# Kernel optimization log

Hardware: AMD Instinct MI355X
Metric: run time of the kernel (lower is better)

## Reference

```python
import jax, jax.numpy as jnp
import numpy as np

WINDOW = 8
HEADS = 16
HIDDEN = 256
EMBED = HIDDEN * WINDOW          # 2048
HEAD_DIM = EMBED // HEADS        # 128
BATCH = 8
SEQ = 4096                       # multiple of WINDOW
GROUP = SEQ // WINDOW            # 512


def _indices():
    # index_one[i*g + j] = j*w + i  (residue-class grouping permutation)
    i = np.arange(WINDOW)
    j = np.arange(GROUP)
    index_one = (j[None, :] * WINDOW + i[:, None]).reshape(-1)
    # index_two[i*w + k] = k*g + i  (inverse-style interleave permutation)
    index_two = (np.arange(WINDOW)[None, :] * GROUP + np.arange(GROUP)[:, None]).reshape(-1)
    return jnp.asarray(index_one), jnp.asarray(index_two)


def _attention(M, Wq, Wk, Wv, fc_w, fc_b):
    # M: [N, g, E] with E = heads*head_dim
    N, L, E = M.shape
    x = M.reshape(N, L, HEADS, HEAD_DIM)
    q = jnp.einsum('nlhd,ed->nlhe', x, Wq)
    k = jnp.einsum('nlhd,ed->nlhe', x, Wk)
    v = jnp.einsum('nlhd,ed->nlhe', x, Wv)
    energy = jnp.einsum('nqhd,nkhd->nhqk', q, k)
    attn = jax.nn.softmax(energy / jnp.sqrt(jnp.float32(EMBED)), axis=-1)
    out = jnp.einsum('nhqk,nkhd->nqhd', attn, v).reshape(N, L, E)
    return out @ fc_w.T + fc_b


def setup_inputs() -> dict:
    key = jax.random.key(0)
    ks = jax.random.split(key, 6)
    s = 0.02
    return {
        'M': jax.random.normal(ks[0], (BATCH, SEQ, HIDDEN), jnp.float32),
        'Wq': jax.random.normal(ks[1], (HEAD_DIM, HEAD_DIM), jnp.float32) * s,
        'Wk': jax.random.normal(ks[2], (HEAD_DIM, HEAD_DIM), jnp.float32) * s,
        'Wv': jax.random.normal(ks[3], (HEAD_DIM, HEAD_DIM), jnp.float32) * s,
        'fc_w': jax.random.normal(ks[4], (EMBED, EMBED), jnp.float32) * s,
        'fc_b': jax.random.normal(ks[5], (EMBED,), jnp.float32) * s,
        'device': 0,
    }


def reference(M, Wq, Wk, Wv, fc_w, fc_b, device):
    del device  # unused, mirrors torch signature
    index_one, index_two = _indices()
    N, S, H = M.shape
    w, g = WINDOW, GROUP
    for b in range(w):
        idx = (index_one - b) % S
        M = M[:, idx]                                             # gather permute
        # segmentation step 1: [N, w*g, H] -> [N, g, w*H]
        M = M.reshape(N, w, g, H).transpose(0, 2, 1, 3).reshape(N, g, w * H)
        M = _attention(M, Wq, Wk, Wv, fc_w, fc_b)
        # segmentation step 2: [N, g, w*H] -> [N, w*g, H]
        M = M.reshape(N, g, w, H).transpose(0, 2, 1, 3).reshape(N, w * g, H)
        # index_two rotated once per iteration after the first -> roll by -b
        M = M[:, jnp.roll(index_two, -b)]
    return M[:, :S]
```

## Files before the change

### kernel.cpp

```cpp
#include <hip/hip_runtime.h>
#include <stdint.h>

typedef unsigned short u16;
typedef unsigned int u32;
typedef __bf16 bf16x8 __attribute__((ext_vector_type(8)));
typedef float f32x4 __attribute__((ext_vector_type(4)));
typedef float f32x16 __attribute__((ext_vector_type(16)));
typedef u16 u16x4 __attribute__((ext_vector_type(4)));
typedef u16 u16x8 __attribute__((ext_vector_type(8)));

#define MFMA16(a, b, c) __builtin_amdgcn_mfma_f32_16x16x32_bf16(a, b, c, 0, 0, 0)
#define MFMA32(a, b, c) __builtin_amdgcn_mfma_f32_32x32x16_bf16(a, b, c, 0, 0, 0)

__device__ __forceinline__ u16 f2bf(float f) {
  u32 u = __builtin_bit_cast(u32, f);
  u += 0x7FFFu + ((u >> 16) & 1u);
  return (u16)(u >> 16);
}

__device__ __forceinline__ bf16x8 ld16(const u16* p) {
  return __builtin_bit_cast(bf16x8, *(const uint4*)p);
}

__device__ __forceinline__ void gl_lds(const u16* src, u16* lds) {
  __builtin_amdgcn_global_load_lds(
      (const __attribute__((address_space(1))) u32*)src,
      (__attribute__((address_space(3))) u32*)lds, 16, 0, 0);
}

__global__ __launch_bounds__(256) void convert_weights(
    const float* __restrict__ Wq, const float* __restrict__ Wk,
    const float* __restrict__ Wv, const float* __restrict__ fcw,
    u16* __restrict__ wq_b, u16* __restrict__ wk_b, u16* __restrict__ wv_b,
    u16* __restrict__ fcw_b) {
  int bx = blockIdx.x, tid = threadIdx.x;
  if (bx < 4096) {
    int i = (bx * 256 + tid) * 4;
    float4 f = *(const float4*)&fcw[i];
    u16x4 o = {f2bf(f.x), f2bf(f.y), f2bf(f.z), f2bf(f.w)};
    *(u16x4*)&fcw_b[i] = o;
  } else {
    int i = ((bx - 4096) * 256 + tid) * 4;
    const float sc = 0.022097086912079612f;
    float4 q = *(const float4*)&Wq[i];
    u16x4 oq = {f2bf(q.x * sc), f2bf(q.y * sc), f2bf(q.z * sc), f2bf(q.w * sc)};
    *(u16x4*)&wq_b[i] = oq;
    float4 k = *(const float4*)&Wk[i];
    u16x4 ok = {f2bf(k.x), f2bf(k.y), f2bf(k.z), f2bf(k.w)};
    *(u16x4*)&wk_b[i] = ok;
    float4 v = *(const float4*)&Wv[i];
    u16x4 ov = {f2bf(v.x), f2bf(v.y), f2bf(v.z), f2bf(v.w)};
    *(u16x4*)&wv_b[i] = ov;
  }
}

__global__ __launch_bounds__(384) void qkv_kernel(
    const float* __restrict__ src, const u16* __restrict__ wq,
    const u16* __restrict__ wk, const u16* __restrict__ wvw,
    u16* __restrict__ Q, u16* __restrict__ K, u16* __restrict__ Vt, int bsh) {
  __shared__ u16 X[64 * 136];
  int jt = blockIdx.x, h = blockIdx.y, n = blockIdx.z;
  int tid = threadIdx.x;
  int i0 = h >> 1, c0 = (h & 1) * 128;
  for (int it = 0; it < 3; ++it) {
    int c = tid + it * 384;
    if (c < 1024) {
      int row = c >> 4, seg = c & 15;
      int j = jt * 64 + row;
      int pos = (8 * j + i0 - bsh) & 4095;
      const float* g = src + ((size_t)n * 4096 + pos) * 256 + c0 + seg * 8;
      float4 f0 = *(const float4*)g;
      float4 f1 = *(const float4*)(g + 4);
      u16x8 v = {f2bf(f0.x), f2bf(f0.y), f2bf(f0.z), f2bf(f0.w),
                 f2bf(f1.x), f2bf(f1.y), f2bf(f1.z), f2bf(f1.w)};
      *(u16x8*)&X[row * 136 + seg * 8] = v;
    }
  }
  __syncthreads();
  int wv = tid >> 6, ln = tid & 63;
  int mat = wv >> 1;
  int cbase = (wv & 1) * 64;
  const u16* W = (mat == 0) ? wq : (mat == 1) ? wk : wvw;
  int lr = ln & 15, lg = ln >> 4;
  f32x4 acc[4][4] = {};
#pragma unroll
  for (int kt = 0; kt < 4; ++kt) {
    bf16x8 a[4], b[4];
#pragma unroll
    for (int mt = 0; mt < 4; ++mt)
      a[mt] = ld16(&X[(mt * 16 + lr) * 136 + kt * 32 + lg * 8]);
#pragma unroll
    for (int nc = 0; nc < 4; ++nc)
      b[nc] = ld16(&W[(cbase + nc * 16 + lr) * 128 + kt * 32 + lg * 8]);
#pragma unroll
    for (int mt = 0; mt < 4; ++mt)
#pragma unroll
      for (int nc = 0; nc < 4; ++nc)
        acc[mt][nc] = MFMA16(a[mt], b[nc], acc[mt][nc]);
  }
  size_t nh = (size_t)(n * 16 + h);
  if (mat < 2) {
    u16* dst = (mat == 0 ? Q : K) + nh * 512 * 128;
#pragma unroll
    for (int mt = 0; mt < 4; ++mt)
#pragma unroll
      for (int nc = 0; nc < 4; ++nc) {
        int col = cbase + nc * 16 + lr;
        int jb = jt * 64 + mt * 16 + lg * 4;
#pragma unroll
        for (int r = 0; r < 4; ++r)
          dst[(size_t)(jb + r) * 128 + col] = f2bf(acc[mt][nc][r]);
      }
  } else {
    u16* dst = Vt + nh * 128 * 512;
#pragma unroll
    for (int mt = 0; mt < 4; ++mt)
#pragma unroll
      for (int nc = 0; nc < 4; ++nc) {
        int col = cbase + nc * 16 + lr;
        int jb = jt * 64 + mt * 16 + lg * 4;
        u16x4 pk = {f2bf(acc[mt][nc][0]), f2bf(acc[mt][nc][1]),
                    f2bf(acc[mt][nc][2]), f2bf(acc[mt][nc][3])};
        *(u16x4*)&dst[(size_t)col * 512 + jb] = pk;
      }
  }
}

__global__ __launch_bounds__(256, 2) void attn_kernel(
    const u16* __restrict__ Q, const u16* __restrict__ K,
    const u16* __restrict__ Vt, u16* __restrict__ O) {
  __shared__ u16 KL[2][64 * 128];
  __shared__ u16 VL[2][128 * 64];
  int flat = blockIdx.x;
  int xcd = flat & 7, idx = flat >> 3;
  int gl = idx & 15, qt = idx >> 4;
  int g = xcd | (gl << 3);
  int h = g & 15, n = g >> 4;
  int tid = threadIdx.x, wv = tid >> 6, ln = tid & 63;
  int l31 = ln & 31, hh = ln >> 5;
  size_t nh = (size_t)(n * 16 + h);
  int q0 = qt * 128 + wv * 32;
  const u16* Qb = Q + ((size_t)nh * 512 + q0) * 128;
  const u16* Kb = K + (size_t)nh * 512 * 128;
  const u16* Vb = Vt + (size_t)nh * 128 * 512;

  bf16x8 qf[8];
#pragma unroll
  for (int kt = 0; kt < 8; ++kt)
    qf[kt] = ld16(&Qb[l31 * 128 + kt * 16 + hh * 8]);

  int l16 = ln & 15, l8 = ln & 7;
  int rK[4], cK[4], rV[4], cV[4];
#pragma unroll
  for (int i = 0; i < 4; ++i) {
    int s = wv * 4 + i;
    rK[i] = 4 * s + (ln >> 4);
    cK[i] = (l16 ^ (rK[i] & 15)) * 8;
    rV[i] = 8 * s + (ln >> 3);
    cV[i] = (l8 ^ (rV[i] & 7)) * 8;
  }

#pragma unroll
  for (int i = 0; i < 4; ++i) {
    int s = wv * 4 + i;
    gl_lds(&Kb[(size_t)rK[i] * 128 + cK[i]], &KL[0][s * 512]);
    gl_lds(&Vb[(size_t)rV[i] * 512 + 0 * 64 + cV[i]], &VL[0][s * 512]);
  }
  __syncthreads();

  f32x16 o[4] = {};
  float m = -1e30f, l = 0.f;

  for (int kv = 0; kv < 8; ++kv) {
    int cur = kv & 1;
    if (kv < 7) {
      int nxt = cur ^ 1;
      const u16* kp = Kb + (size_t)(kv + 1) * 64 * 128;
#pragma unroll
      for (int i = 0; i < 4; ++i) {
        int s = wv * 4 + i;
        gl_lds(&kp[(size_t)rK[i] * 128 + cK[i]], &KL[nxt][s * 512]);
        gl_lds(&Vb[(size_t)rV[i] * 512 + (kv + 1) * 64 + cV[i]], &VL[nxt][s * 512]);
      }
    }
    f32x16 s[2] = {};
#pragma unroll
    for (int kb = 0; kb < 2; ++kb)
#pragma unroll
      for (int kt = 0; kt < 8; ++kt) {
        int row = kb * 32 + l31;
        int slot = (2 * kt + hh) ^ (row & 15);
        bf16x8 a = ld16(&KL[cur][row * 128 + slot * 8]);
        s[kb] = MFMA32(a, qf[kt], s[kb]);
      }
    float mx[8];
#pragma unroll
    for (int i = 0; i < 8; ++i)
      mx[i] = fmaxf(fmaxf(s[0][2 * i], s[0][2 * i + 1]),
                    fmaxf(s[1][2 * i], s[1][2 * i + 1]));
    float pm = fmaxf(fmaxf(fmaxf(mx[0], mx[1]), fmaxf(mx[2], mx[3])),
                     fmaxf(fmaxf(mx[4], mx[5]), fmaxf(mx[6], mx[7])));
    pm = fmaxf(pm, __shfl_xor(pm, 32));
    if (!__all(pm <= m + 8.f)) {
      float nm = fmaxf(m, pm);
      float al = __expf(m - nm);
      l *= al;
      m = nm;
#pragma unroll
      for (int r = 0; r < 16; ++r) {
        int qr = (r & 3) + 8 * (r >> 2) + 4 * hh;
        float av = __shfl(al, (ln & 32) | qr, 64);
        o[0][r] *= av; o[1][r] *= av; o[2][r] *= av; o[3][r] *= av;
      }
    }
#pragma unroll
    for (int kb = 0; kb < 2; ++kb)
#pragma unroll
      for (int r = 0; r < 16; ++r) s[kb][r] = __expf(s[kb][r] - m);
    float sm[8];
#pragma unroll
    for (int i = 0; i < 8; ++i)
      sm[i] = (s[0][2 * i] + s[0][2 * i + 1]) + (s[1][2 * i] + s[1][2 * i + 1]);
    float rs = ((sm[0] + sm[1]) + (sm[2] + sm[3])) +
               ((sm[4] + sm[5]) + (sm[6] + sm[7]));
    rs += __shfl_xor(rs, 32);
    l += rs;
    bf16x8 pa[4];
#pragma unroll
    for (int ks = 0; ks < 4; ++ks) {
      const int kb = ks >> 1, r0 = 8 * (ks & 1);
      u32 wA, wB, wC, wD;
      asm("v_cvt_pk_bf16_f32 %0, %1, %2" : "=v"(wA) : "v"(s[kb][r0 + 0]), "v"(s[kb][r0 + 1]));
      asm("v_cvt_pk_bf16_f32 %0, %1, %2" : "=v"(wB) : "v"(s[kb][r0 + 2]), "v"(s[kb][r0 + 3]));
      asm("v_cvt_pk_bf16_f32 %0, %1, %2" : "=v"(wC) : "v"(s[kb][r0 + 4]), "v"(s[kb][r0 + 5]));
      asm("v_cvt_pk_bf16_f32 %0, %1, %2" : "=v"(wD) : "v"(s[kb][r0 + 6]), "v"(s[kb][r0 + 7]));
      asm("v_permlane32_swap_b32 %0, %1" : "+v"(wA), "+v"(wC));
      asm("v_permlane32_swap_b32 %0, %1" : "+v"(wB), "+v"(wD));
      uint4 ww = {wA, wB, wC, wD};
      pa[ks] = __builtin_bit_cast(bf16x8, ww);
    }
#pragma unroll
    for (int ks = 0; ks < 4; ++ks)
#pragma unroll
      for (int nb = 0; nb < 4; ++nb) {
        int row = nb * 32 + l31;
        int slot = (2 * ks + hh) ^ (row & 7);
        bf16x8 bv = ld16(&VL[cur][row * 64 + slot * 8]);
        o[nb] = MFMA32(pa[ks], bv, o[nb]);
      }
    if (kv < 7) __syncthreads();
  }
  float inv = 1.f / l;
#pragma unroll
  for (int r = 0; r < 16; ++r) {
    int qr = (r & 3) + 8 * (r >> 2) + 4 * hh;
    float iv = __shfl(inv, (ln & 32) | qr, 64);
    int row = q0 + qr;
    u16* dst = O + ((size_t)n * 512 + row) * 2048 + h * 128;
    dst[0 * 32 + l31] = f2bf(o[0][r] * iv);
    dst[1 * 32 + l31] = f2bf(o[1][r] * iv);
    dst[2 * 32 + l31] = f2bf(o[2][r] * iv);
    dst[3 * 32 + l31] = f2bf(o[3][r] * iv);
  }
}

__global__ __launch_bounds__(256) void fc_kernel(
    const u16* __restrict__ A, const u16* __restrict__ Bw,
    const float* __restrict__ bias, float* __restrict__ dout, int bsh) {
  __shared__ u16 Al[128 * 32];
  __shared__ u16 Bl[128 * 32];
  int bn = blockIdx.x, bm = blockIdx.y;
  int tid = threadIdx.x, wv = tid >> 6, ln = tid & 63;
  int lr = ln & 15, lg = ln >> 4;
  int R0 = bm * 128, C0 = bn * 128;
  int wr = (wv & 1) * 64, wc = (wv >> 1) * 64;
  int lrow = ln >> 2, lseg = ln & 3;
  f32x4 acc[4][4] = {};
  for (int ks = 0; ks < 64; ++ks) {
    int k0 = ks * 32;
#pragma unroll
    for (int ch = wv; ch < 8; ch += 4) {
      const u16* ga = A + (size_t)(R0 + ch * 16 + lrow) * 2048 + k0 + lseg * 8;
      gl_lds(ga, &Al[ch * 512]);
      const u16* gb = Bw + (size_t)(C0 + ch * 16 + lrow) * 2048 + k0 + lseg * 8;
      gl_lds(gb, &Bl[ch * 512]);
    }
    __syncthreads();
    bf16x8 a[4], b[4];
#pragma unroll
    for (int mt = 0; mt < 4; ++mt)
      a[mt] = ld16(&Al[(wr + mt * 16 + lr) * 32 + lg * 8]);
#pragma unroll
    for (int nc = 0; nc < 4; ++nc)
      b[nc] = ld16(&Bl[(wc + nc * 16 + lr) * 32 + lg * 8]);
#pragma unroll
    for (int mt = 0; mt < 4; ++mt)
#pragma unroll
      for (int nc = 0; nc < 4; ++nc)
        acc[mt][nc] = MFMA16(a[mt], b[nc], acc[mt][nc]);
    __syncthreads();
  }
#pragma unroll
  for (int nc = 0; nc < 4; ++nc) {
    int e = C0 + wc + nc * 16 + lr;
    float bv = bias[e];
    int i = e >> 8, cc = e & 255;
#pragma unroll
    for (int mt = 0; mt < 4; ++mt)
#pragma unroll
      for (int r = 0; r < 4; ++r) {
        int row = R0 + wr + mt * 16 + lg * 4 + r;
        int nn = row >> 9, j = row & 511;
        int pos = (8 * j + i - bsh) & 4095;
        dout[((size_t)nn * 4096 + pos) * 256 + cc] = acc[mt][nc][r] + bv;
      }
  }
}

extern "C" void kernel_launch(void* const* d_in, const int* in_sizes, int n_in,
                              void* d_out, int out_size, void* d_ws, size_t ws_size,
                              hipStream_t stream) {
  const float* M = (const float*)d_in[0];
  const float* Wq = (const float*)d_in[1];
  const float* Wk = (const float*)d_in[2];
  const float* Wv = (const float*)d_in[3];
  const float* fcw = (const float*)d_in[4];
  const float* fcb = (const float*)d_in[5];
  float* out = (float*)d_out;
  char* ws = (char*)d_ws;
  u16* wq_b = (u16*)(ws + (0 << 10));
  u16* wk_b = (u16*)(ws + (32 << 10));
  u16* wv_b = (u16*)(ws + (64 << 10));
  u16* fcw_b = (u16*)(ws + (128 << 10));
  u16* Qb = (u16*)(ws + ((size_t)16 << 20));
  u16* Kb = (u16*)(ws + ((size_t)32 << 20));
  u16* Vtb = (u16*)(ws + ((size_t)48 << 20));
  u16* Ab = (u16*)(ws + ((size_t)64 << 20));

  convert_weights<<<4112, 256, 0, stream>>>(Wq, Wk, Wv, fcw, wq_b, wk_b, wv_b, fcw_b);
  for (int b = 0; b < 8; ++b) {
    const float* src = (b == 0) ? M : out;
    qkv_kernel<<<dim3(8, 16, 8), 384, 0, stream>>>(src, wq_b, wk_b, wv_b, Qb, Kb, Vtb, b);
    attn_kernel<<<512, 256, 0, stream>>>(Qb, Kb, Vtb, Ab);
    fc_kernel<<<dim3(16, 32), 256, 0, stream>>>(Ab, fcw_b, fcb, out, b);
  }
}
```

Measured before the change: 810.0 us.

## Double-buffer FC GEMM with larger tiles, merge QKV head pairs, add MFMA priorities

The FC GEMM kernel now uses 512-thread blocks with 128x256 tiles. It double-buffers LDS with swizzled layouts and splits each k-step into two phases with partial vmcnt waits, so global loads overlap MFMA work. The QKV kernel processes both heads of a row residue in one 768-thread block, loading the full 256-wide row once instead of twice. s_setprio hints are also added around MFMA sections in attention and FC. These changes trade more LDS and register pressure, and more complex barrier ordering, for fewer redundant loads and better latency hiding.

```diff
diff --git a/kernel.cpp b/kernel.cpp
--- a/kernel.cpp
+++ b/kernel.cpp
@@ -54,32 +54,29 @@
   }
 }
 
-__global__ __launch_bounds__(384) void qkv_kernel(
+__global__ __launch_bounds__(768) void qkv_kernel(
     const float* __restrict__ src, const u16* __restrict__ wq,
     const u16* __restrict__ wk, const u16* __restrict__ wvw,
     u16* __restrict__ Q, u16* __restrict__ K, u16* __restrict__ Vt, int bsh) {
-  __shared__ u16 X[64 * 136];
-  int jt = blockIdx.x, h = blockIdx.y, n = blockIdx.z;
+  __shared__ u16 X[64 * 264];
+  int jt = blockIdx.x, i0 = blockIdx.y, n = blockIdx.z;
   int tid = threadIdx.x;
-  int i0 = h >> 1, c0 = (h & 1) * 128;
-  for (int it = 0; it < 3; ++it) {
-    int c = tid + it * 384;
-    if (c < 1024) {
-      int row = c >> 4, seg = c & 15;
-      int j = jt * 64 + row;
-      int pos = (8 * j + i0 - bsh) & 4095;
-      const float* g = src + ((size_t)n * 4096 + pos) * 256 + c0 + seg * 8;
-      float4 f0 = *(const float4*)g;
-      float4 f1 = *(const float4*)(g + 4);
-      u16x8 v = {f2bf(f0.x), f2bf(f0.y), f2bf(f0.z), f2bf(f0.w),
-                 f2bf(f1.x), f2bf(f1.y), f2bf(f1.z), f2bf(f1.w)};
-      *(u16x8*)&X[row * 136 + seg * 8] = v;
+#pragma unroll
+  for (int r = 0; r < 6; ++r) {
+    int idx = tid + r * 768;
+    if (idx < 4096) {
+      int row = idx >> 6, c4 = idx & 63;
+      int pos = (8 * (jt * 64 + row) + i0 - bsh) & 4095;
+      float4 f = *(const float4*)&src[((size_t)n * 4096 + pos) * 256 + c4 * 4];
+      u16x4 v = {f2bf(f.x), f2bf(f.y), f2bf(f.z), f2bf(f.w)};
+      *(u16x4*)&X[row * 264 + c4 * 4] = v;
     }
   }
   __syncthreads();
-  int wv = tid >> 6, ln = tid & 63;
-  int mat = wv >> 1;
-  int cbase = (wv & 1) * 64;
+  int wvid = tid >> 6, ln = tid & 63;
+  int mat = wvid >> 2, hc = wvid & 3;
+  int hh = hc >> 1, cb = (hc & 1) * 64;
+  int h = i0 * 2 + hh, xc = hh * 128;
   const u16* W = (mat == 0) ? wq : (mat == 1) ? wk : wvw;
   int lr = ln & 15, lg = ln >> 4;
   f32x4 acc[4][4] = {};
@@ -88,10 +85,10 @@
     bf16x8 a[4], b[4];
 #pragma unroll
     for (int mt = 0; mt < 4; ++mt)
-      a[mt] = ld16(&X[(mt * 16 + lr) * 136 + kt * 32 + lg * 8]);
+      a[mt] = ld16(&X[(mt * 16 + lr) * 264 + xc + kt * 32 + lg * 8]);
 #pragma unroll
     for (int nc = 0; nc < 4; ++nc)
-      b[nc] = ld16(&W[(cbase + nc * 16 + lr) * 128 + kt * 32 + lg * 8]);
+      b[nc] = ld16(&W[(cb + nc * 16 + lr) * 128 + kt * 32 + lg * 8]);
 #pragma unroll
     for (int mt = 0; mt < 4; ++mt)
 #pragma unroll
@@ -105,7 +102,7 @@
     for (int mt = 0; mt < 4; ++mt)
 #pragma unroll
       for (int nc = 0; nc < 4; ++nc) {
-        int col = cbase + nc * 16 + lr;
+        int col = cb + nc * 16 + lr;
         int jb = jt * 64 + mt * 16 + lg * 4;
 #pragma unroll
         for (int r = 0; r < 4; ++r)
@@ -117,7 +114,7 @@
     for (int mt = 0; mt < 4; ++mt)
 #pragma unroll
       for (int nc = 0; nc < 4; ++nc) {
-        int col = cbase + nc * 16 + lr;
+        int col = cb + nc * 16 + lr;
         int jb = jt * 64 + mt * 16 + lg * 4;
         u16x4 pk = {f2bf(acc[mt][nc][0]), f2bf(acc[mt][nc][1]),
                     f2bf(acc[mt][nc][2]), f2bf(acc[mt][nc][3])};
@@ -184,6 +181,7 @@
       }
     }
     f32x16 s[2] = {};
+    __builtin_amdgcn_s_setprio(1);
 #pragma unroll
     for (int kb = 0; kb < 2; ++kb)
 #pragma unroll
@@ -193,6 +191,7 @@
         bf16x8 a = ld16(&KL[cur][row * 128 + slot * 8]);
         s[kb] = MFMA32(a, qf[kt], s[kb]);
       }
+    __builtin_amdgcn_s_setprio(0);
     float mx[8];
 #pragma unroll
     for (int i = 0; i < 8; ++i)
@@ -239,6 +238,7 @@
       uint4 ww = {wA, wB, wC, wD};
       pa[ks] = __builtin_bit_cast(bf16x8, ww);
     }
+    __builtin_amdgcn_s_setprio(1);
 #pragma unroll
     for (int ks = 0; ks < 4; ++ks)
 #pragma unroll
@@ -248,6 +248,7 @@
         bf16x8 bv = ld16(&VL[cur][row * 64 + slot * 8]);
         o[nb] = MFMA32(pa[ks], bv, o[nb]);
       }
+    __builtin_amdgcn_s_setprio(0);
     if (kv < 7) __syncthreads();
   }
   float inv = 1.f / l;
@@ -264,41 +265,102 @@
   }
 }
 
-__global__ __launch_bounds__(256) void fc_kernel(
+__global__ __launch_bounds__(512, 2) void fc_kernel(
     const u16* __restrict__ A, const u16* __restrict__ Bw,
     const float* __restrict__ bias, float* __restrict__ dout, int bsh) {
-  __shared__ u16 Al[128 * 32];
-  __shared__ u16 Bl[128 * 32];
+  __shared__ u16 AL[2][128 * 32];
+  __shared__ u16 BL[2][256 * 32];
   int bn = blockIdx.x, bm = blockIdx.y;
   int tid = threadIdx.x, wv = tid >> 6, ln = tid & 63;
   int lr = ln & 15, lg = ln >> 4;
-  int R0 = bm * 128, C0 = bn * 128;
-  int wr = (wv & 1) * 64, wc = (wv >> 1) * 64;
-  int lrow = ln >> 2, lseg = ln & 3;
+  int R0 = bm * 128, C0 = bn * 256;
+  int wr = (wv >> 2) * 64, wc = (wv & 3) * 64;
+  int sr = ln >> 2, ss = ln & 3;
+  int trA = wv * 16 + sr;
+  int trB0 = wv * 32 + sr, trB1 = wv * 32 + 16 + sr;
+  const u16* gA = A + (size_t)(R0 + trA) * 2048 + (ss ^ (trA & 3)) * 8;
+  const u16* gB0 = Bw + (size_t)(C0 + trB0) * 2048 + (ss ^ (trB0 & 3)) * 8;
+  const u16* gB1 = Bw + (size_t)(C0 + trB1) * 2048 + (ss ^ (trB1 & 3)) * 8;
+  int aoff[4], boff[4];
+#pragma unroll
+  for (int i = 0; i < 4; ++i) {
+    int ta = wr + i * 16 + lr;
+    aoff[i] = ta * 32 + ((lg ^ (ta & 3)) * 8);
+    int tb = wc + i * 16 + lr;
+    boff[i] = tb * 32 + ((lg ^ (tb & 3)) * 8);
+  }
   f32x4 acc[4][4] = {};
-  for (int ks = 0; ks < 64; ++ks) {
-    int k0 = ks * 32;
-#pragma unroll
-    for (int ch = wv; ch < 8; ch += 4) {
-      const u16* ga = A + (size_t)(R0 + ch * 16 + lrow) * 2048 + k0 + lseg * 8;
-      gl_lds(ga, &Al[ch * 512]);
-      const u16* gb = Bw + (size_t)(C0 + ch * 16 + lrow) * 2048 + k0 + lseg * 8;
-      gl_lds(gb, &Bl[ch * 512]);
-    }
-    __syncthreads();
-    bf16x8 a[4], b[4];
-#pragma unroll
-    for (int mt = 0; mt < 4; ++mt)
-      a[mt] = ld16(&Al[(wr + mt * 16 + lr) * 32 + lg * 8]);
-#pragma unroll
-    for (int nc = 0; nc < 4; ++nc)
-      b[nc] = ld16(&Bl[(wc + nc * 16 + lr) * 32 + lg * 8]);
-#pragma unroll
-    for (int mt = 0; mt < 4; ++mt)
-#pragma unroll
-      for (int nc = 0; nc < 4; ++nc)
-        acc[mt][nc] = MFMA16(a[mt], b[nc], acc[mt][nc]);
-    __syncthreads();
+
+  gl_lds(gA, &AL[0][wv * 512]);
+  gl_lds(gB0, &BL[0][wv * 1024]);
+  gl_lds(gB1, &BL[0][wv * 1024 + 512]);
+  asm volatile("s_waitcnt vmcnt(0)" ::: "memory");
+  __builtin_amdgcn_s_barrier();
+
+  for (int t = 0; t < 63; ++t) {
+    int c = t & 1, nx = c ^ 1;
+    int k0 = (t + 1) * 32;
+    gl_lds(gA + k0, &AL[nx][wv * 512]);
+    gl_lds(gB0 + k0, &BL[nx][wv * 1024]);
+    asm volatile("s_waitcnt vmcnt(2)" ::: "memory");
+    __builtin_amdgcn_s_barrier();
+    bf16x8 b0 = ld16(&BL[c][boff[0]]), b1 = ld16(&BL[c][boff[1]]);
+    bf16x8 b2 = ld16(&BL[c][boff[2]]), b3 = ld16(&BL[c][boff[3]]);
+    {
+      bf16x8 a0 = ld16(&AL[c][aoff[0]]), a1 = ld16(&AL[c][aoff[1]]);
+      __builtin_amdgcn_s_setprio(1);
+      acc[0][0] = MFMA16(a0, b0, acc[0][0]);
+      acc[0][1] = MFMA16(a0, b1, acc[0][1]);
+      acc[0][2] = MFMA16(a0, b2, acc[0][2]);
+      acc[0][3] = MFMA16(a0, b3, acc[0][3]);
+      acc[1][0] = MFMA16(a1, b0, acc[1][0]);
+      acc[1][1] = MFMA16(a1, b1, acc[1][1]);
+      acc[1][2] = MFMA16(a1, b2, acc[1][2]);
+      acc[1][3] = MFMA16(a1, b3, acc[1][3]);
+      __builtin_amdgcn_s_setprio(0);
+    }
+    __builtin_amdgcn_s_barrier();
+    gl_lds(gB1 + k0, &BL[nx][wv * 1024 + 512]);
+    {
+      bf16x8 a2 = ld16(&AL[c][aoff[2]]), a3 = ld16(&AL[c][aoff[3]]);
+      __builtin_amdgcn_s_barrier();
+      __builtin_amdgcn_s_setprio(1);
+      acc[2][0] = MFMA16(a2, b0, acc[2][0]);
+      acc[2][1] = MFMA16(a2, b1, acc[2][1]);
+      acc[2][2] = MFMA16(a2, b2, acc[2][2]);
+      acc[2][3] = MFMA16(a2, b3, acc[2][3]);
+      acc[3][0] = MFMA16(a3, b0, acc[3][0]);
+      acc[3][1] = MFMA16(a3, b1, acc[3][1]);
+      acc[3][2] = MFMA16(a3, b2, acc[3][2]);
+      acc[3][3] = MFMA16(a3, b3, acc[3][3]);
+      __builtin_amdgcn_s_setprio(0);
+    }
+    __builtin_amdgcn_s_barrier();
+  }
+  {
+    const int c = 1;
+    asm volatile("s_waitcnt vmcnt(0)" ::: "memory");
+    __builtin_amdgcn_s_barrier();
+    bf16x8 b0 = ld16(&BL[c][boff[0]]), b1 = ld16(&BL[c][boff[1]]);
+    bf16x8 b2 = ld16(&BL[c][boff[2]]), b3 = ld16(&BL[c][boff[3]]);
+    bf16x8 a0 = ld16(&AL[c][aoff[0]]), a1 = ld16(&AL[c][aoff[1]]);
+    bf16x8 a2 = ld16(&AL[c][aoff[2]]), a3 = ld16(&AL[c][aoff[3]]);
+    acc[0][0] = MFMA16(a0, b0, acc[0][0]);
+    acc[0][1] = MFMA16(a0, b1, acc[0][1]);
+    acc[0][2] = MFMA16(a0, b2, acc[0][2]);
+    acc[0][3] = MFMA16(a0, b3, acc[0][3]);
+    acc[1][0] = MFMA16(a1, b0, acc[1][0]);
+    acc[1][1] = MFMA16(a1, b1, acc[1][1]);
+    acc[1][2] = MFMA16(a1, b2, acc[1][2]);
+    acc[1][3] = MFMA16(a1, b3, acc[1][3]);
+    acc[2][0] = MFMA16(a2, b0, acc[2][0]);
+    acc[2][1] = MFMA16(a2, b1, acc[2][1]);
+    acc[2][2] = MFMA16(a2, b2, acc[2][2]);
+    acc[2][3] = MFMA16(a2, b3, acc[2][3]);
+    acc[3][0] = MFMA16(a3, b0, acc[3][0]);
+    acc[3][1] = MFMA16(a3, b1, acc[3][1]);
+    acc[3][2] = MFMA16(a3, b2, acc[3][2]);
+    acc[3][3] = MFMA16(a3, b3, acc[3][3]);
   }
 #pragma unroll
   for (int nc = 0; nc < 4; ++nc) {
@@ -340,8 +402,8 @@
   convert_weights<<<4112, 256, 0, stream>>>(Wq, Wk, Wv, fcw, wq_b, wk_b, wv_b, fcw_b);
   for (int b = 0; b < 8; ++b) {
     const float* src = (b == 0) ? M : out;
-    qkv_kernel<<<dim3(8, 16, 8), 384, 0, stream>>>(src, wq_b, wk_b, wv_b, Qb, Kb, Vtb, b);
+    qkv_kernel<<<dim3(8, 8, 8), 768, 0, stream>>>(src, wq_b, wk_b, wv_b, Qb, Kb, Vtb, b);
     attn_kernel<<<512, 256, 0, stream>>>(Qb, Kb, Vtb, Ab);
-    fc_kernel<<<dim3(16, 32), 256, 0, stream>>>(Ab, fcw_b, fcb, out, b);
-  }
-}
+    fc_kernel<<<dim3(8, 32), 512, 0, stream>>>(Ab, fcw_b, fcb, out, b);
+  }
+}
```

Result: slower. 902.4 us (+11.4%).
